# Optimization experiments

Measured on AMD Instinct MI355X. Metric: run time of the kernel, lower is better.

Reference implementation:

```python
import jax, jax.numpy as jnp
import numpy as np

B, D = 500000, 128
UNITS, STACK, NPRED = 4, 12, 2
EPS = 1e-3  # Keras BatchNormalization default epsilon


def setup_inputs() -> dict:
    key = jax.random.key(0)
    ks = jax.random.split(key, 2 * STACK + 4)
    inp = {"x": jax.random.normal(ks[0], (B, D), dtype=jnp.float32)}
    # 12 dense weights with growing input width D + 4*i
    for i in range(STACK):
        inp[f"w{i}"] = jax.random.normal(ks[1 + i], (D + UNITS * i, UNITS), dtype=jnp.float32) * 0.1
    inp["gamma"] = 1.0 + 0.1 * jax.random.normal(ks[STACK + 1], (STACK, UNITS), dtype=jnp.float32)
    inp["beta"] = 0.1 * jax.random.normal(ks[STACK + 2], (STACK, UNITS), dtype=jnp.float32)
    inp["mean"] = 0.1 * jax.random.normal(ks[STACK + 3], (STACK, UNITS), dtype=jnp.float32)
    inp["var"] = 0.5 + jax.random.uniform(ks[2 * STACK], (STACK, UNITS), dtype=jnp.float32)
    inp["wf"] = jax.random.normal(ks[2 * STACK + 1], (D + UNITS * STACK, NPRED), dtype=jnp.float32) * 0.1
    inp["bf"] = jnp.zeros((NPRED,), dtype=jnp.float32)
    return inp


def reference(x, w0, w1, w2, w3, w4, w5, w6, w7, w8, w9, w10, w11,
              gamma, beta, mean, var, wf, bf):
    ws = [w0, w1, w2, w3, w4, w5, w6, w7, w8, w9, w10, w11]
    h = x
    for i in range(STACK):
        y = h @ ws[i]  # [B, 4]
        # inference-mode BatchNorm, fused scale/shift
        scale = gamma[i] * jax.lax.rsqrt(var[i] + EPS)
        y = jax.nn.relu(y * scale + (beta[i] - mean[i] * scale))
        h = jnp.concatenate([y, h], axis=-1)  # width grows by 4
    logits = h @ wf + bf  # [B, 2]
    return jax.nn.softmax(logits, axis=-1)
```

## Files before the change

kernel.cpp:

```cpp
#include <hip/hip_runtime.h>

#define NROWS 500000
#define DD 128
#define NSTACK 12
#define BNEPS 1e-3f
#define NCOL 50
#define TRS 51

typedef float  v2f    __attribute__((ext_vector_type(2)));
typedef float  v4f    __attribute__((ext_vector_type(4)));
typedef float  f32x4  __attribute__((ext_vector_type(4)));
typedef __bf16 bf16x8 __attribute__((ext_vector_type(8)));

__device__ __forceinline__ unsigned short f2bf_rn(float f) {
    unsigned u = __float_as_uint(f);
    return (unsigned short)((u + 0x7FFFu + ((u >> 16) & 1u)) >> 16);
}


__global__ void prep_kernel(
    const float* __restrict__ w0,  const float* __restrict__ w1,
    const float* __restrict__ w2,  const float* __restrict__ w3,
    const float* __restrict__ w4,  const float* __restrict__ w5,
    const float* __restrict__ w6,  const float* __restrict__ w7,
    const float* __restrict__ w8,  const float* __restrict__ w9,
    const float* __restrict__ w10, const float* __restrict__ w11,
    const float* __restrict__ gamma_, const float* __restrict__ beta_,
    const float* __restrict__ mean_,  const float* __restrict__ var_,
    const float* __restrict__ wf,     const float* __restrict__ bfv,
    unsigned short* __restrict__ frag, float* __restrict__ sc,
    float* __restrict__ sh, float* __restrict__ bf2)
{
    const float* ws[NSTACK] = {w0,w1,w2,w3,w4,w5,w6,w7,w8,w9,w10,w11};
    const int f    = blockIdx.x * 256 + threadIdx.x;
    const int j    = f & 7;
    const int lane = (f >> 3) & 63;
    const int nt   = (f >> 9) & 3;
    const int kt   = f >> 11;
    const int k    = kt * 32 + (lane >> 4) * 8 + j;
    const int n    = nt * 16 + (lane & 15);

    float val = 0.f;
    if (n < 48) {
        const int i = n >> 2, u = n & 3;
        val = ws[i][16 * i + 4 * k + u];
    } else if (n < NCOL) {
        val = wf[96 + 2 * k + (n - 48)];
    }
    frag[f] = f2bf_rn(val);

    if (blockIdx.x == 0) {
        if (threadIdx.x < 48) {
            const float s = gamma_[threadIdx.x] * __frsqrt_rn(var_[threadIdx.x] + BNEPS);
            sc[threadIdx.x] = s;
            sh[threadIdx.x] = beta_[threadIdx.x] - mean_[threadIdx.x] * s;
        }
        if (threadIdx.x < 2) bf2[threadIdx.x] = bfv[threadIdx.x];
    }
}

__global__ __launch_bounds__(256, 3) void predict_kernel(
    const float* __restrict__ x,
    const float* __restrict__ w0,  const float* __restrict__ w1,
    const float* __restrict__ w2,  const float* __restrict__ w3,
    const float* __restrict__ w4,  const float* __restrict__ w5,
    const float* __restrict__ w6,  const float* __restrict__ w7,
    const float* __restrict__ w8,  const float* __restrict__ w9,
    const float* __restrict__ w10, const float* __restrict__ w11,
    const float* __restrict__ wf,
    const unsigned short* __restrict__ frag,
    const float* __restrict__ SCg, const float* __restrict__ SHg,
    const float* __restrict__ BFg,
    float* __restrict__ out)
{
    __shared__ __align__(16) float trow[256 * TRS];

    const int tid  = threadIdx.x;
    const int lane = tid & 63;
    const int wv   = tid >> 6;
    const int rowbase = blockIdx.x * 256 + wv * 64;
    const int m = lane & 15;
    const int q = lane >> 4;

    const float* arow[4];
#pragma unroll
    for (int mt = 0; mt < 4; ++mt) {
        int r = rowbase + mt * 16 + m;
        if (r > NROWS - 1) r = NROWS - 1;
        arow[mt] = x + (size_t)r * DD + q * 8;
    }

    f32x4 acc[4][4];
#pragma unroll
    for (int mt = 0; mt < 4; ++mt)
#pragma unroll
        for (int nt = 0; nt < 4; ++nt) acc[mt][nt] = (f32x4){0.f, 0.f, 0.f, 0.f};

    v4f pa0[4], pa1[4];
#pragma unroll
    for (int mt = 0; mt < 4; ++mt) {
        pa0[mt] = *(const v4f*)(arow[mt]);
        pa1[mt] = *(const v4f*)(arow[mt] + 4);
    }

#pragma unroll
    for (int kt = 0; kt < 4; ++kt) {
        bf16x8 bfrag[4];
#pragma unroll
        for (int nt = 0; nt < 4; ++nt)
            bfrag[nt] = *(const bf16x8*)(frag + (((kt * 4 + nt) * 64 + lane) << 3));

        v4f na0[4], na1[4];
        if (kt < 3) {
#pragma unroll
            for (int mt = 0; mt < 4; ++mt) {
                na0[mt] = *(const v4f*)(arow[mt] + (kt + 1) * 32);
                na1[mt] = *(const v4f*)(arow[mt] + (kt + 1) * 32 + 4);
            }
        }

#pragma unroll
        for (int mt = 0; mt < 4; ++mt) {
            bf16x8 av;
#pragma unroll
            for (int e = 0; e < 4; ++e) {
                av[e]     = (__bf16)pa0[mt][e];
                av[4 + e] = (__bf16)pa1[mt][e];
            }
#pragma unroll
            for (int nt = 0; nt < 4; ++nt)
                acc[mt][nt] = __builtin_amdgcn_mfma_f32_16x16x32_bf16(
                    av, bfrag[nt], acc[mt][nt], 0, 0, 0);
        }

        if (kt < 3) {
#pragma unroll
            for (int mt = 0; mt < 4; ++mt) {
                pa0[mt] = na0[mt];
                pa1[mt] = na1[mt];
            }
        }
    }

    float* tr = &trow[wv * 64 * TRS];
#pragma unroll
    for (int mt = 0; mt < 4; ++mt)
#pragma unroll
        for (int nt = 0; nt < 4; ++nt) {
            const int c = nt * 16 + m;
            if (c < NCOL) {
#pragma unroll
                for (int r = 0; r < 4; ++r)
                    tr[(mt * 16 + q * 4 + r) * TRS + c] = acc[mt][nt][r];
            }
        }

    const float* myT = &trow[(wv * 64 + lane) * TRS];
    const float* ws[NSTACK] = {w0,w1,w2,w3,w4,w5,w6,w7,w8,w9,w10,w11};

    v2f y2[NSTACK * 2];
#pragma unroll
    for (int i = 0; i < NSTACK; ++i) {
        v2f a01 = *(const v2f*)(myT + 4 * i);
        v2f a23 = *(const v2f*)(myT + 4 * i + 2);
        const float* wsi = ws[i];
#pragma unroll
        for (int mr = 0; mr < 4 * i; ++mr) {
            const int yi = (i - 1 - (mr >> 2)) * 4 + (mr & 3);
            const float hvs = y2[yi >> 1][yi & 1];
            const v2f hv2 = {hvs, hvs};
            a01 += hv2 * (*(const v2f*)(wsi + 4 * mr));
            a23 += hv2 * (*(const v2f*)(wsi + 4 * mr + 2));
        }
        const v2f sc01 = *(const v2f*)(SCg + 4 * i);
        const v2f sc23 = *(const v2f*)(SCg + 4 * i + 2);
        const v2f sh01 = *(const v2f*)(SHg + 4 * i);
        const v2f sh23 = *(const v2f*)(SHg + 4 * i + 2);
        v2f r01 = a01 * sc01 + sh01;
        v2f r23 = a23 * sc23 + sh23;
        r01.x = fmaxf(r01.x, 0.f); r01.y = fmaxf(r01.y, 0.f);
        r23.x = fmaxf(r23.x, 0.f); r23.y = fmaxf(r23.y, 0.f);
        y2[2 * i]     = r01;
        y2[2 * i + 1] = r23;
    }

    v2f l01 = *(const v2f*)(myT + 48) + *(const v2f*)BFg;
#pragma unroll
    for (int mr = 0; mr < 48; ++mr) {
        const int yi = (11 - (mr >> 2)) * 4 + (mr & 3);
        const float hvs = y2[yi >> 1][yi & 1];
        const v2f hv2 = {hvs, hvs};
        l01 += hv2 * (*(const v2f*)(wf + 2 * mr));
    }

    const float mx = fmaxf(l01.x, l01.y);
    const float e0 = __expf(l01.x - mx);
    const float e1 = __expf(l01.y - mx);
    const float inv = 1.0f / (e0 + e1);

    const int row = rowbase + lane;
    if (row < NROWS)
        *(v2f*)(out + (size_t)row * 2) = (v2f){e0 * inv, e1 * inv};
}

extern "C" void kernel_launch(void* const* d_in, const int* in_sizes, int n_in,
                              void* d_out, int out_size, void* d_ws, size_t ws_size,
                              hipStream_t stream) {
    const float* x   = (const float*)d_in[0];
    const float* w0  = (const float*)d_in[1];
    const float* w1  = (const float*)d_in[2];
    const float* w2  = (const float*)d_in[3];
    const float* w3  = (const float*)d_in[4];
    const float* w4  = (const float*)d_in[5];
    const float* w5  = (const float*)d_in[6];
    const float* w6  = (const float*)d_in[7];
    const float* w7  = (const float*)d_in[8];
    const float* w8  = (const float*)d_in[9];
    const float* w9  = (const float*)d_in[10];
    const float* w10 = (const float*)d_in[11];
    const float* w11 = (const float*)d_in[12];
    const float* gm  = (const float*)d_in[13];
    const float* bt  = (const float*)d_in[14];
    const float* mn  = (const float*)d_in[15];
    const float* vr  = (const float*)d_in[16];
    const float* wf  = (const float*)d_in[17];
    const float* bf  = (const float*)d_in[18];
    float* out = (float*)d_out;

    unsigned short* frag = (unsigned short*)d_ws;
    float* SCg = (float*)((char*)d_ws + 16384);
    float* SHg = (float*)((char*)d_ws + 16576);
    float* BFg = (float*)((char*)d_ws + 16768);

    hipLaunchKernelGGL(prep_kernel, dim3(32), dim3(256), 0, stream,
                       w0, w1, w2, w3, w4, w5, w6, w7, w8, w9, w10, w11,
                       gm, bt, mn, vr, wf, bf, frag, SCg, SHg, BFg);

    dim3 block(256);
    dim3 grid((NROWS + 255) / 256);
    hipLaunchKernelGGL(predict_kernel, grid, block, 0, stream,
                       x, w0, w1, w2, w3, w4, w5, w6, w7, w8, w9, w10, w11,
                       wf, frag, SCg, SHg, BFg, out);
}
```

Before: 390.7 us.

## Process two 64-row tiles per wave, prefetching the second during the first tail

Each block now handles 512 rows: every wave runs the MFMA GEMM on its first 64-row tile, issues the global loads for the second tile, and runs the serial dense-stack tail of the first tile while those loads are in flight. The tail's inner FMA chains are also split into two interleaved accumulators to shorten dependency chains. The grid shrinks by half, so there is less launch and setup overhead per row, but there are fewer blocks to balance across CUs and register pressure rises from the extra in-flight loads. Rounding changes slightly because of the reassociated sums.

```diff
diff --git a/kernel.cpp b/kernel.cpp
--- a/kernel.cpp
+++ b/kernel.cpp
@@ -6,6 +6,7 @@
 #define BNEPS 1e-3f
 #define NCOL 50
 #define TRS 51
+#define RPB 512
 
 typedef float  v2f    __attribute__((ext_vector_type(2)));
 typedef float  v4f    __attribute__((ext_vector_type(4)));
@@ -57,6 +58,150 @@
         }
         if (threadIdx.x < 2) bf2[threadIdx.x] = bfv[threadIdx.x];
     }
+}
+
+
+__device__ __forceinline__ void set_arows(const float* __restrict__ x, int rowbase,
+                                          int m, int q, const float** arow)
+{
+#pragma unroll
+    for (int mt = 0; mt < 4; ++mt) {
+        int r = rowbase + mt * 16 + m;
+        if (r > NROWS - 1) r = NROWS - 1;
+        arow[mt] = x + (size_t)r * DD + q * 8;
+    }
+}
+
+__device__ __forceinline__ void prefetch_kt0(const float* const* arow, v4f* pa0, v4f* pa1)
+{
+#pragma unroll
+    for (int mt = 0; mt < 4; ++mt) {
+        pa0[mt] = *(const v4f*)(arow[mt]);
+        pa1[mt] = *(const v4f*)(arow[mt] + 4);
+    }
+}
+
+__device__ __forceinline__ void gemm64(const float* const* arow, v4f* pa0, v4f* pa1,
+                                       const unsigned short* __restrict__ frag,
+                                       int lane, f32x4 (*acc)[4])
+{
+#pragma unroll
+    for (int mt = 0; mt < 4; ++mt)
+#pragma unroll
+        for (int nt = 0; nt < 4; ++nt) acc[mt][nt] = (f32x4){0.f, 0.f, 0.f, 0.f};
+
+#pragma unroll
+    for (int kt = 0; kt < 4; ++kt) {
+        bf16x8 bfrag[4];
+#pragma unroll
+        for (int nt = 0; nt < 4; ++nt)
+            bfrag[nt] = *(const bf16x8*)(frag + (((kt * 4 + nt) * 64 + lane) << 3));
+
+        v4f na0[4], na1[4];
+        if (kt < 3) {
+#pragma unroll
+            for (int mt = 0; mt < 4; ++mt) {
+                na0[mt] = *(const v4f*)(arow[mt] + (kt + 1) * 32);
+                na1[mt] = *(const v4f*)(arow[mt] + (kt + 1) * 32 + 4);
+            }
+        }
+
+#pragma unroll
+        for (int mt = 0; mt < 4; ++mt) {
+            bf16x8 av;
+#pragma unroll
+            for (int e = 0; e < 4; ++e) {
+                av[e]     = (__bf16)pa0[mt][e];
+                av[4 + e] = (__bf16)pa1[mt][e];
+            }
+#pragma unroll
+            for (int nt = 0; nt < 4; ++nt)
+                acc[mt][nt] = __builtin_amdgcn_mfma_f32_16x16x32_bf16(
+                    av, bfrag[nt], acc[mt][nt], 0, 0, 0);
+        }
+
+        if (kt < 3) {
+#pragma unroll
+            for (int mt = 0; mt < 4; ++mt) {
+                pa0[mt] = na0[mt];
+                pa1[mt] = na1[mt];
+            }
+        }
+    }
+}
+
+__device__ __forceinline__ void transpose64(const f32x4 (*acc)[4], float* tr, int m, int q)
+{
+#pragma unroll
+    for (int mt = 0; mt < 4; ++mt)
+#pragma unroll
+        for (int nt = 0; nt < 4; ++nt) {
+            const int c = nt * 16 + m;
+            if (c < NCOL) {
+#pragma unroll
+                for (int r = 0; r < 4; ++r)
+                    tr[(mt * 16 + q * 4 + r) * TRS + c] = acc[mt][nt][r];
+            }
+        }
+}
+
+__device__ __forceinline__ void tail64(const float* myT, const float* const* ws,
+                                       const float* __restrict__ SCg,
+                                       const float* __restrict__ SHg,
+                                       const float* __restrict__ BFg,
+                                       const float* __restrict__ wf,
+                                       float* __restrict__ out, int row)
+{
+    v2f y2[NSTACK * 2];
+#pragma unroll
+    for (int i = 0; i < NSTACK; ++i) {
+        v2f ac01[2], ac23[2];
+        ac01[0] = *(const v2f*)(myT + 4 * i);
+        ac23[0] = *(const v2f*)(myT + 4 * i + 2);
+        ac01[1] = (v2f){0.f, 0.f};
+        ac23[1] = (v2f){0.f, 0.f};
+        const float* wsi = ws[i];
+#pragma unroll
+        for (int mr = 0; mr < 4 * i; ++mr) {
+            const int yi = (i - 1 - (mr >> 2)) * 4 + (mr & 3);
+            const float hvs = y2[yi >> 1][yi & 1];
+            const v2f hv2 = {hvs, hvs};
+            ac01[mr & 1] += hv2 * (*(const v2f*)(wsi + 4 * mr));
+            ac23[mr & 1] += hv2 * (*(const v2f*)(wsi + 4 * mr + 2));
+        }
+        const v2f a01 = ac01[0] + ac01[1];
+        const v2f a23 = ac23[0] + ac23[1];
+        const v2f sc01 = *(const v2f*)(SCg + 4 * i);
+        const v2f sc23 = *(const v2f*)(SCg + 4 * i + 2);
+        const v2f sh01 = *(const v2f*)(SHg + 4 * i);
+        const v2f sh23 = *(const v2f*)(SHg + 4 * i + 2);
+        v2f r01 = a01 * sc01 + sh01;
+        v2f r23 = a23 * sc23 + sh23;
+        r01.x = fmaxf(r01.x, 0.f); r01.y = fmaxf(r01.y, 0.f);
+        r23.x = fmaxf(r23.x, 0.f); r23.y = fmaxf(r23.y, 0.f);
+        y2[2 * i]     = r01;
+        y2[2 * i + 1] = r23;
+    }
+
+    v2f lc[2];
+    lc[0] = *(const v2f*)(myT + 48) + *(const v2f*)BFg;
+    lc[1] = (v2f){0.f, 0.f};
+#pragma unroll
+    for (int mr = 0; mr < 48; ++mr) {
+        const int yi = (11 - (mr >> 2)) * 4 + (mr & 3);
+        const float hvs = y2[yi >> 1][yi & 1];
+        const v2f hv2 = {hvs, hvs};
+        lc[mr & 1] += hv2 * (*(const v2f*)(wf + 2 * mr));
+    }
+    const v2f l01 = lc[0] + lc[1];
+
+    const float mx = fmaxf(l01.x, l01.y);
+    const float e0 = __expf(l01.x - mx);
+    const float e1 = __expf(l01.y - mx);
+    const float inv = 1.0f / (e0 + e1);
+
+    if (row < NROWS)
+        *(v2f*)(out + (size_t)row * 2) = (v2f){e0 * inv, e1 * inv};
 }
 
 __global__ __launch_bounds__(256, 3) void predict_kernel(
@@ -78,129 +223,33 @@
     const int tid  = threadIdx.x;
     const int lane = tid & 63;
     const int wv   = tid >> 6;
-    const int rowbase = blockIdx.x * 256 + wv * 64;
     const int m = lane & 15;
     const int q = lane >> 4;
-
-    const float* arow[4];
-#pragma unroll
-    for (int mt = 0; mt < 4; ++mt) {
-        int r = rowbase + mt * 16 + m;
-        if (r > NROWS - 1) r = NROWS - 1;
-        arow[mt] = x + (size_t)r * DD + q * 8;
-    }
-
-    f32x4 acc[4][4];
-#pragma unroll
-    for (int mt = 0; mt < 4; ++mt)
-#pragma unroll
-        for (int nt = 0; nt < 4; ++nt) acc[mt][nt] = (f32x4){0.f, 0.f, 0.f, 0.f};
-
-    v4f pa0[4], pa1[4];
-#pragma unroll
-    for (int mt = 0; mt < 4; ++mt) {
-        pa0[mt] = *(const v4f*)(arow[mt]);
-        pa1[mt] = *(const v4f*)(arow[mt] + 4);
-    }
-
-#pragma unroll
-    for (int kt = 0; kt < 4; ++kt) {
-        bf16x8 bfrag[4];
-#pragma unroll
-        for (int nt = 0; nt < 4; ++nt)
-            bfrag[nt] = *(const bf16x8*)(frag + (((kt * 4 + nt) * 64 + lane) << 3));
-
-        v4f na0[4], na1[4];
-        if (kt < 3) {
-#pragma unroll
-            for (int mt = 0; mt < 4; ++mt) {
-                na0[mt] = *(const v4f*)(arow[mt] + (kt + 1) * 32);
-                na1[mt] = *(const v4f*)(arow[mt] + (kt + 1) * 32 + 4);
-            }
-        }
-
-#pragma unroll
-        for (int mt = 0; mt < 4; ++mt) {
-            bf16x8 av;
-#pragma unroll
-            for (int e = 0; e < 4; ++e) {
-                av[e]     = (__bf16)pa0[mt][e];
-                av[4 + e] = (__bf16)pa1[mt][e];
-            }
-#pragma unroll
-            for (int nt = 0; nt < 4; ++nt)
-                acc[mt][nt] = __builtin_amdgcn_mfma_f32_16x16x32_bf16(
-                    av, bfrag[nt], acc[mt][nt], 0, 0, 0);
-        }
-
-        if (kt < 3) {
-#pragma unroll
-            for (int mt = 0; mt < 4; ++mt) {
-                pa0[mt] = na0[mt];
-                pa1[mt] = na1[mt];
-            }
-        }
-    }
-
     float* tr = &trow[wv * 64 * TRS];
-#pragma unroll
-    for (int mt = 0; mt < 4; ++mt)
-#pragma unroll
-        for (int nt = 0; nt < 4; ++nt) {
-            const int c = nt * 16 + m;
-            if (c < NCOL) {
-#pragma unroll
-                for (int r = 0; r < 4; ++r)
-                    tr[(mt * 16 + q * 4 + r) * TRS + c] = acc[mt][nt][r];
-            }
-        }
-
     const float* myT = &trow[(wv * 64 + lane) * TRS];
     const float* ws[NSTACK] = {w0,w1,w2,w3,w4,w5,w6,w7,w8,w9,w10,w11};
 
-    v2f y2[NSTACK * 2];
-#pragma unroll
-    for (int i = 0; i < NSTACK; ++i) {
-        v2f a01 = *(const v2f*)(myT + 4 * i);
-        v2f a23 = *(const v2f*)(myT + 4 * i + 2);
-        const float* wsi = ws[i];
-#pragma unroll
-        for (int mr = 0; mr < 4 * i; ++mr) {
-            const int yi = (i - 1 - (mr >> 2)) * 4 + (mr & 3);
-            const float hvs = y2[yi >> 1][yi & 1];
-            const v2f hv2 = {hvs, hvs};
-            a01 += hv2 * (*(const v2f*)(wsi + 4 * mr));
-            a23 += hv2 * (*(const v2f*)(wsi + 4 * mr + 2));
-        }
-        const v2f sc01 = *(const v2f*)(SCg + 4 * i);
-        const v2f sc23 = *(const v2f*)(SCg + 4 * i + 2);
-        const v2f sh01 = *(const v2f*)(SHg + 4 * i);
-        const v2f sh23 = *(const v2f*)(SHg + 4 * i + 2);
-        v2f r01 = a01 * sc01 + sh01;
-        v2f r23 = a23 * sc23 + sh23;
-        r01.x = fmaxf(r01.x, 0.f); r01.y = fmaxf(r01.y, 0.f);
-        r23.x = fmaxf(r23.x, 0.f); r23.y = fmaxf(r23.y, 0.f);
-        y2[2 * i]     = r01;
-        y2[2 * i + 1] = r23;
-    }
-
-    v2f l01 = *(const v2f*)(myT + 48) + *(const v2f*)BFg;
-#pragma unroll
-    for (int mr = 0; mr < 48; ++mr) {
-        const int yi = (11 - (mr >> 2)) * 4 + (mr & 3);
-        const float hvs = y2[yi >> 1][yi & 1];
-        const v2f hv2 = {hvs, hvs};
-        l01 += hv2 * (*(const v2f*)(wf + 2 * mr));
-    }
-
-    const float mx = fmaxf(l01.x, l01.y);
-    const float e0 = __expf(l01.x - mx);
-    const float e1 = __expf(l01.y - mx);
-    const float inv = 1.0f / (e0 + e1);
-
-    const int row = rowbase + lane;
-    if (row < NROWS)
-        *(v2f*)(out + (size_t)row * 2) = (v2f){e0 * inv, e1 * inv};
+    const int rb0 = blockIdx.x * RPB + wv * 64;
+    const int rb1 = rb0 + 256;
+
+    f32x4 acc[4][4];
+    v4f pa0[4], pa1[4];
+
+    const float* arow0[4];
+    set_arows(x, rb0, m, q, arow0);
+    prefetch_kt0(arow0, pa0, pa1);
+    gemm64(arow0, pa0, pa1, frag, lane, acc);
+    transpose64(acc, tr, m, q);
+
+    const float* arow1[4];
+    set_arows(x, rb1, m, q, arow1);
+    prefetch_kt0(arow1, pa0, pa1);
+
+    tail64(myT, ws, SCg, SHg, BFg, wf, out, rb0 + lane);
+
+    gemm64(arow1, pa0, pa1, frag, lane, acc);
+    transpose64(acc, tr, m, q);
+    tail64(myT, ws, SCg, SHg, BFg, wf, out, rb1 + lane);
 }
 
 extern "C" void kernel_launch(void* const* d_in, const int* in_sizes, int n_in,
@@ -237,7 +286,7 @@
                        gm, bt, mn, vr, wf, bf, frag, SCg, SHg, BFg);
 
     dim3 block(256);
-    dim3 grid((NROWS + 255) / 256);
+    dim3 grid((NROWS + RPB - 1) / RPB);
     hipLaunchKernelGGL(predict_kernel, grid, block, 0, stream,
                        x, w0, w1, w2, w3, w4, w5, w6, w7, w8, w9, w10, w11,
                        wf, frag, SCg, SHg, BFg, out);
```

After: 394.9 us. About the same (+1.1%).
